# Kernel tuning notes

Measured on AMD Instinct MI355X. Metric: run time of the kernel, lower is better.

## Reference

```python
import jax, jax.numpy as jnp
import numpy as np

HEADS = 16
DIM_HEAD = 64

def setup_inputs() -> dict:
    key = jax.random.key(0)
    ks = jax.random.split(key, 7)
    B, Nq, Dq = 4, 2048, 1024
    Nk, Dc = 1024, 768
    inner = HEADS * DIM_HEAD  # 1024
    sq = 1.0 / np.sqrt(Dq)
    sc = 1.0 / np.sqrt(Dc)
    si = 1.0 / np.sqrt(inner)
    return {
        "x": jax.random.normal(ks[0], (B, Nq, Dq), dtype=jnp.float32),
        "context": jax.random.normal(ks[1], (B, Nk, Dc), dtype=jnp.float32),
        "Wq": jax.random.normal(ks[2], (Dq, inner), dtype=jnp.float32) * sq,
        "Wk": jax.random.normal(ks[3], (Dc, inner), dtype=jnp.float32) * sc,
        "Wv": jax.random.normal(ks[4], (Dc, inner), dtype=jnp.float32) * sc,
        "Wo": jax.random.normal(ks[5], (inner, Dq), dtype=jnp.float32) * si,
        "bo": jax.random.normal(ks[6], (Dq,), dtype=jnp.float32) * 0.01,
    }

def reference(x, context, Wq, Wk, Wv, Wo, bo):
    B, Nq, _ = x.shape
    Nk = context.shape[1]
    h, dh = HEADS, DIM_HEAD
    # projections (no bias on q/k/v, matching nn.Linear(bias=False))
    q = (x @ Wq).reshape(B, Nq, h, dh)        # [B,Nq,h,dh]
    k = (context @ Wk).reshape(B, Nk, h, dh)  # [B,Nk,h,dh]
    v = (context @ Wv).reshape(B, Nk, h, dh)
    scale = 1.0 / jnp.sqrt(jnp.asarray(dh, dtype=x.dtype))
    # scores: [B,h,Nq,Nk]
    scores = jnp.einsum('bqhd,bkhd->bhqk', q, k) * scale
    attn = jax.nn.softmax(scores, axis=-1)
    out = jnp.einsum('bhqk,bkhd->bqhd', attn, v).reshape(B, Nq, h * dh)
    return out @ Wo + bo
```

## Files before the change

kernel.cpp:

```cpp
#include <hip/hip_runtime.h>

typedef __bf16 bf16;
typedef __bf16 bf16x2 __attribute__((ext_vector_type(2)));
typedef __bf16 bf16x4 __attribute__((ext_vector_type(4)));
typedef __bf16 bf16x8 __attribute__((ext_vector_type(8)));
typedef float f32x4 __attribute__((ext_vector_type(4)));

#define MFMA(a, b, c) __builtin_amdgcn_mfma_f32_16x16x32_bf16(a, b, c, 0, 0, 0)

#define GLD16(gptr, ldsptr)                                                        \
  __builtin_amdgcn_global_load_lds(                                                \
      (const __attribute__((address_space(1))) unsigned int*)(gptr),               \
      (__attribute__((address_space(3))) unsigned int*)(ldsptr), 16, 0, 0)

union I4B8 { int4 i; bf16x8 v; };
union HI { bf16x2 h; int i; };

__global__ __launch_bounds__(256) void prep_k(const float* __restrict__ x, bf16* __restrict__ xb,
                                              const float* __restrict__ ctx, bf16* __restrict__ ctxb,
                                              const float* __restrict__ Wq, bf16* __restrict__ WqT,
                                              const float* __restrict__ Wk, bf16* __restrict__ WkvT,
                                              const float* __restrict__ Wv,
                                              const float* __restrict__ Wo, bf16* __restrict__ WoT) {
  __shared__ float t[32][33];
  const int bid = blockIdx.x;
  if (bid < 5632) {
    const float* in; bf16* out; size_t i;
    if (bid < 4096) { in = x; out = xb; i = ((size_t)bid * 256 + threadIdx.x) * 8; }
    else { in = ctx; out = ctxb; i = ((size_t)(bid - 4096) * 256 + threadIdx.x) * 8; }
    const float4 a = *(const float4*)(in + i);
    const float4 b = *(const float4*)(in + i + 4);
    bf16x8 o;
    o[0] = (bf16)a.x; o[1] = (bf16)a.y; o[2] = (bf16)a.z; o[3] = (bf16)a.w;
    o[4] = (bf16)b.x; o[5] = (bf16)b.y; o[6] = (bf16)b.z; o[7] = (bf16)b.w;
    *(bf16x8*)(out + i) = o;
    return;
  }
  const int tt = bid - 5632;
  const int z = tt >> 10, rem = tt & 1023;
  const float* in; bf16* out; int R; float sc = 1.0f;
  if (z == 0)      { in = Wq; out = WqT;                R = 1024; sc = 0.18033688f; }
  else if (z == 1) { in = Wk; out = WkvT;               R = 768; }
  else if (z == 2) { in = Wv; out = WkvT + 1024 * 768;  R = 768; }
  else             { in = Wo; out = WoT;                R = 1024; }
  const int c0 = (rem & 31) * 32, r0 = (rem >> 5) * 32;
  if (r0 >= R) return;
  const int tx = threadIdx.x & 31, ty = threadIdx.x >> 5;
#pragma unroll
  for (int i = 0; i < 4; i++)
    t[ty + i * 8][tx] = in[(size_t)(r0 + ty + i * 8) * 1024 + c0 + tx];
  __syncthreads();
#pragma unroll
  for (int i = 0; i < 4; i++)
    out[(size_t)(c0 + ty + i * 8) * R + r0 + tx] = (bf16)(t[tx][ty + i * 8] * sc);
}

__device__ __forceinline__ void ld_af(bf16x8 (&af)[4][2], const bf16* Ls, int base,
                                      int wm, int c, int q, int swz) {
#pragma unroll
  for (int mi = 0; mi < 4; mi++) {
    const int rr = wm * 64 + mi * 16 + c;
#pragma unroll
    for (int kk = 0; kk < 2; kk++)
      af[mi][kk] = *(const bf16x8*)&Ls[base + rr * 64 + ((kk * 32 + q * 8) ^ swz)];
  }
}
__device__ __forceinline__ void ld_bb(bf16x8 (&bb)[2][2], const bf16* Ls, int base,
                                      int wn, int c, int q, int swz) {
#pragma unroll
  for (int ni = 0; ni < 2; ni++) {
    const int rn = wn * 32 + ni * 16 + c;
#pragma unroll
    for (int kk = 0; kk < 2; kk++)
      bb[ni][kk] = *(const bf16x8*)&Ls[base + rn * 64 + ((kk * 32 + q * 8) ^ swz)];
  }
}
template <int MODE>
__device__ __forceinline__ void mma16(f32x4 (&pacc)[4][2], const bf16x8 (&af)[4][2],
                                      const bf16x8 (&bb)[2][2]) {
  __builtin_amdgcn_s_setprio(1);
#pragma unroll
  for (int mi = 0; mi < 4; mi++)
#pragma unroll
    for (int ni = 0; ni < 2; ni++)
#pragma unroll
      for (int kk = 0; kk < 2; kk++) {
        if constexpr (MODE == 2)
          pacc[mi][ni] = MFMA(af[mi][kk], bb[ni][kk], pacc[mi][ni]);
        else
          pacc[mi][ni] = MFMA(bb[ni][kk], af[mi][kk], pacc[mi][ni]);
      }
  __builtin_amdgcn_s_setprio(0);
}

template <int MODE>
__device__ __forceinline__ void gemm256(const bf16* __restrict__ A,
                                        const bf16* __restrict__ Bt,
                                        int K, int m0, int n0,
                                        void* __restrict__ C0,
                                        const float* __restrict__ bias,
                                        bf16* Ls) {
  const int tid = threadIdx.x;
  const int lane = tid & 63, w = tid >> 6;
  const int wm = w >> 2, wn = w & 3;
  const int q = lane >> 4, c = lane & 15;
  const int swz = (c & 7) * 8;

  const int rl = tid >> 3, seg = tid & 7;
  const bf16* Ag = A + (size_t)(m0 + rl) * K + ((seg ^ (rl & 7)) * 8);
  const bf16* Bg = Bt + (size_t)(n0 + rl) * K + ((seg ^ (rl & 7)) * 8);
  const size_t K64 = (size_t)K * 64, K128 = (size_t)K * 128;
  const int ws = w * 512;

  f32x4 acc[2][2][4][2] = {};

  GLD16(Ag,              &Ls[0 + ws]);
  GLD16(Ag + K64,        &Ls[4096 + ws]);
  GLD16(Ag + K128,       &Ls[8192 + ws]);
  GLD16(Ag + K128 + K64, &Ls[12288 + ws]);
  GLD16(Bg,              &Ls[32768 + ws]);
  GLD16(Bg + K64,        &Ls[32768 + 4096 + ws]);
  GLD16(Bg + K128,       &Ls[32768 + 8192 + ws]);
  GLD16(Bg + K128 + K64, &Ls[32768 + 12288 + ws]);

  int cur = 0;
  for (int k0 = 0; k0 < K; k0 += 64) {
    const int nxt = cur ^ 1;
    const size_t kn = (size_t)((k0 + 64 < K) ? k0 + 64 : k0);
    const int Ab = cur * 16384, Bb = 32768 + cur * 16384;
    const int An = nxt * 16384, Bn = 32768 + nxt * 16384;

    bf16x8 af[4][2], b0[2][2], b1[2][2];

    asm volatile("s_waitcnt vmcnt(2)" ::: "memory");
    asm volatile("s_barrier" ::: "memory");
    GLD16(Ag + kn,       &Ls[An + ws]);
    GLD16(Ag + kn + K64, &Ls[An + 4096 + ws]);
    ld_af(af, Ls, Ab, wm, c, q, swz);
    ld_bb(b0, Ls, Bb, wn, c, q, swz);
    mma16<MODE>(acc[0][0], af, b0);

    asm volatile("s_waitcnt vmcnt(2)" ::: "memory");
    asm volatile("s_barrier" ::: "memory");
    GLD16(Ag + kn + K128,       &Ls[An + 8192 + ws]);
    GLD16(Ag + kn + K128 + K64, &Ls[An + 12288 + ws]);
    ld_bb(b1, Ls, Bb + 8192, wn, c, q, swz);
    mma16<MODE>(acc[0][1], af, b1);

    asm volatile("s_barrier" ::: "memory");
    GLD16(Bg + kn,       &Ls[Bn + ws]);
    GLD16(Bg + kn + K64, &Ls[Bn + 4096 + ws]);
    ld_af(af, Ls, Ab + 8192, wm, c, q, swz);
    mma16<MODE>(acc[1][0], af, b0);

    asm volatile("s_barrier" ::: "memory");
    GLD16(Bg + kn + K128,       &Ls[Bn + 8192 + ws]);
    GLD16(Bg + kn + K128 + K64, &Ls[Bn + 12288 + ws]);
    mma16<MODE>(acc[1][1], af, b1);

    cur = nxt;
  }
  asm volatile("s_waitcnt vmcnt(0)" ::: "memory");

  if constexpr (MODE == 0 || MODE == 1) {
#pragma unroll
    for (int h = 0; h < 2; h++)
#pragma unroll
      for (int g = 0; g < 2; g++)
#pragma unroll
        for (int ni = 0; ni < 2; ni++) {
          const int col = n0 + g * 128 + wn * 32 + ni * 16 + q * 4;
          float4 bv4 = {};
          if constexpr (MODE == 1) bv4 = *(const float4*)&bias[col];
#pragma unroll
          for (int mi = 0; mi < 4; mi++) {
            const int row = m0 + h * 128 + wm * 64 + mi * 16 + c;
            if constexpr (MODE == 0) {
              bf16x4 vv;
#pragma unroll
              for (int r2 = 0; r2 < 4; r2++) vv[r2] = (bf16)acc[h][g][mi][ni][r2];
              *(bf16x4*)&((bf16*)C0)[(size_t)row * 1024 + col] = vv;
            } else {
              f32x4 vv;
              vv[0] = acc[h][g][mi][ni][0] + bv4.x; vv[1] = acc[h][g][mi][ni][1] + bv4.y;
              vv[2] = acc[h][g][mi][ni][2] + bv4.z; vv[3] = acc[h][g][mi][ni][3] + bv4.w;
              *(f32x4*)&((float*)C0)[(size_t)row * 1024 + col] = vv;
            }
          }
        }
  } else {
#pragma unroll
    for (int h = 0; h < 2; h++)
#pragma unroll
      for (int g = 0; g < 2; g++)
#pragma unroll
        for (int ni = 0; ni < 2; ni++) {
          const int col = n0 + g * 128 + wn * 32 + ni * 16 + c;
#pragma unroll
          for (int mi = 0; mi < 4; mi++) {
            const int rbase = m0 + h * 128 + wm * 64 + mi * 16 + q * 4;
            const int b = rbase >> 10, key = rbase & 1023;
            bf16* VT = (bf16*)C0;
            const int hh = col >> 6, d = col & 63;
            const int kl = key & 63;
            const int pkey = (key & ~63) | (kl & 32) | ((kl & 12) << 1) | ((kl & 16) >> 2);
            bf16x4 vv;
#pragma unroll
            for (int r2 = 0; r2 < 4; r2++) vv[r2] = (bf16)acc[h][g][mi][ni][r2];
            *(bf16x4*)&VT[((size_t)(b * 16 + hh) * 64 + d) * 1024 + pkey] = vv;
          }
        }
  }
}

__global__ __launch_bounds__(512) void proj_k(const bf16* __restrict__ xb,
                                              const bf16* __restrict__ ctxb,
                                              const bf16* __restrict__ WqT,
                                              const bf16* __restrict__ WkvT,
                                              bf16* __restrict__ Q,
                                              bf16* __restrict__ Kp,
                                              bf16* __restrict__ VT) {
  extern __shared__ __align__(16) bf16 Ls[];
  const int bid = blockIdx.x;
  if (bid < 128) {
    const int x = bid & 7, i = bid >> 3;
    const int rt = x * 4 + (i >> 2), ct = i & 3;
    gemm256<0>(xb, WqT, 1024, rt * 256, ct * 256, Q, nullptr, Ls);
  } else if (bid < 192) {
    const int t = bid - 128, x = t & 7, i = t >> 3;
    const int rt = x * 2 + (i >> 2), ct = i & 3;
    gemm256<0>(ctxb, WkvT, 768, rt * 256, ct * 256, Kp, nullptr, Ls);
  } else {
    const int t = bid - 192, x = t & 7, i = t >> 3;
    const int rt = x * 2 + (i >> 2), ct = i & 3;
    gemm256<2>(ctxb, WkvT + (size_t)1024 * 768, 768, rt * 256, ct * 256, VT, nullptr, Ls);
  }
}

__device__ __forceinline__ void gemm_body_out(const bf16* __restrict__ A,
                                              const bf16* __restrict__ Bt,
                                              int K, int m0, int n0,
                                              float* __restrict__ C0,
                                              const float* __restrict__ bias,
                                              bf16* As, bf16* Bs) {
  const int tid = threadIdx.x;
  const int lane = tid & 63, wave = tid >> 6;
  const int wm = wave >> 1, wn = wave & 1;
  const int q = lane >> 4, c = lane & 15;

  f32x4 acc[4][4] = {};
  const int r = tid >> 3;
  const int col8 = ((tid & 7) * 8) ^ ((r & 7) * 8);
  const bf16* Ag = A + (size_t)(m0 + r) * K + col8;
  const bf16* Bg = Bt + (size_t)(n0 + r) * K + col8;
  const size_t K32 = (size_t)K * 32;
  bf16* AsW = As + wave * 512;
  bf16* BsW = Bs + wave * 512;
  const int swz = (c & 7) * 8;

  for (int k0 = 0; k0 < K; k0 += 64) {
    __syncthreads();
    GLD16(Ag + k0,            AsW);
    GLD16(Ag + k0 + K32,      AsW + 2048);
    GLD16(Ag + k0 + 2 * K32,  AsW + 4096);
    GLD16(Ag + k0 + 3 * K32,  AsW + 6144);
    GLD16(Bg + k0,            BsW);
    GLD16(Bg + k0 + K32,      BsW + 2048);
    GLD16(Bg + k0 + 2 * K32,  BsW + 4096);
    GLD16(Bg + k0 + 3 * K32,  BsW + 6144);
    __syncthreads();
#pragma unroll
    for (int kk = 0; kk < 2; kk++) {
      const int cx = (kk * 32 + q * 8) ^ swz;
      bf16x8 af[4], bfr[4];
#pragma unroll
      for (int mi = 0; mi < 4; mi++)
        af[mi] = *(const bf16x8*)&As[(wm * 64 + mi * 16 + c) * 64 + cx];
#pragma unroll
      for (int ni = 0; ni < 4; ni++)
        bfr[ni] = *(const bf16x8*)&Bs[(wn * 64 + ni * 16 + c) * 64 + cx];
      __builtin_amdgcn_s_setprio(1);
#pragma unroll
      for (int mi = 0; mi < 4; mi++)
#pragma unroll
        for (int ni = 0; ni < 4; ni++)
          acc[mi][ni] = MFMA(bfr[ni], af[mi], acc[mi][ni]);
      __builtin_amdgcn_s_setprio(0);
    }
  }

#pragma unroll
  for (int ni = 0; ni < 4; ni++) {
    const int col = n0 + wn * 64 + ni * 16 + q * 4;
    float4 bv4 = *(const float4*)&bias[col];
#pragma unroll
    for (int mi = 0; mi < 4; mi++) {
      const int row = m0 + wm * 64 + mi * 16 + c;
      f32x4 vv;
      vv[0] = acc[mi][ni][0] + bv4.x; vv[1] = acc[mi][ni][1] + bv4.y;
      vv[2] = acc[mi][ni][2] + bv4.z; vv[3] = acc[mi][ni][3] + bv4.w;
      *(f32x4*)&C0[(size_t)row * 1024 + col] = vv;
    }
  }
}

__global__ __launch_bounds__(256) void out_k(const bf16* __restrict__ O,
                                             const bf16* __restrict__ WoT,
                                             float* __restrict__ out,
                                             const float* __restrict__ bo) {
  __shared__ __align__(16) bf16 As[8192];
  __shared__ __align__(16) bf16 Bs[8192];
  const int bid = blockIdx.x;
  const int s = (bid & 7) * 64 + (bid >> 3);
  gemm_body_out(O, WoT, 1024, (s >> 3) * 128, (s & 7) * 128, out, bo, As, Bs);
}

__global__ __launch_bounds__(256, 2) void attn_k(const bf16* __restrict__ Qg,
                                                 const bf16* __restrict__ Kg,
                                                 const bf16* __restrict__ VTg,
                                                 bf16* __restrict__ Og) {
  __shared__ __align__(16) bf16 Ks[2][64][64];
  __shared__ __align__(16) bf16 Vt[2][64][64];
  const int tid = threadIdx.x;
  const int lane = tid & 63, w = tid >> 6;
  const int q = lane >> 4, c = lane & 15;
  const int bid = blockIdx.x;
  const int pair = (bid & 7) * 8 + (bid >> 6);
  const int head = pair & 15, b = pair >> 4;
  const int q0 = ((bid >> 3) & 7) * 256;

  bf16x8 aQ[4][2];
#pragma unroll
  for (int mj = 0; mj < 4; mj++)
#pragma unroll
    for (int ks = 0; ks < 2; ks++)
      aQ[mj][ks] = *(const bf16x8*)(Qg + (size_t)(b * 2048 + q0 + w * 64 + mj * 16 + c) * 1024 +
                                    head * 64 + ks * 32 + q * 8);

  f32x4 o[4][4] = {};
  f32x4 ol[4] = {};
  bf16x8 vone;
#pragma unroll
  for (int i = 0; i < 8; i++) vone[i] = (bf16)1.0f;

  const int srow = tid >> 2, sc = tid & 3;
  const int ws0 = ((2 * sc) ^ (srow & 7)) * 8;
  const int ws1 = ((2 * sc + 1) ^ (srow & 7)) * 8;
  const int rsw = c & 7;
  const bf16* Kbase = Kg + (size_t)(b * 1024 + srow) * 1024 + head * 64 + sc * 16;
  const bf16* Vbase = VTg + ((size_t)(b * 16 + head) * 64 + srow) * 1024 + sc * 16;

  bf16x8 rk0 = *(const bf16x8*)(Kbase);
  bf16x8 rk1 = *(const bf16x8*)(Kbase + 8);
  bf16x8 rv0 = *(const bf16x8*)(Vbase);
  bf16x8 rv1 = *(const bf16x8*)(Vbase + 8);
  *(bf16x8*)&Ks[0][srow][ws0] = rk0;
  *(bf16x8*)&Ks[0][srow][ws1] = rk1;
  *(bf16x8*)&Vt[0][srow][ws0] = rv0;
  *(bf16x8*)&Vt[0][srow][ws1] = rv1;
  __syncthreads();

  for (int kt = 0; kt < 16; kt++) {
    const int cur = kt & 1, nxt = cur ^ 1;
    if (kt < 15) {
      const size_t ko = (size_t)(kt + 1) * 65536;
      const int vo = (kt + 1) * 64;
      rk0 = *(const bf16x8*)(Kbase + ko);
      rk1 = *(const bf16x8*)(Kbase + ko + 8);
      rv0 = *(const bf16x8*)(Vbase + vo);
      rv1 = *(const bf16x8*)(Vbase + vo + 8);
    }

    f32x4 st[4][4] = {};
#pragma unroll
    for (int ks = 0; ks < 2; ks++) {
      bf16x8 ak[4];
#pragma unroll
      for (int ni = 0; ni < 4; ni++)
        ak[ni] = *(const bf16x8*)&Ks[cur][ni * 16 + c][((ks * 4 + q) ^ rsw) * 8];
      __builtin_amdgcn_s_setprio(1);
#pragma unroll
      for (int mj = 0; mj < 4; mj++)
#pragma unroll
        for (int ni = 0; ni < 4; ni++)
          st[mj][ni] = MFMA(ak[ni], aQ[mj][ks], st[mj][ni]);
      __builtin_amdgcn_s_setprio(0);
    }

    int pk[4][4][2];
#pragma unroll
    for (int mj = 0; mj < 4; mj++)
#pragma unroll
      for (int ni = 0; ni < 4; ni++) {
        float p0 = __builtin_amdgcn_exp2f(st[mj][ni][0]);
        float p1 = __builtin_amdgcn_exp2f(st[mj][ni][1]);
        float p2 = __builtin_amdgcn_exp2f(st[mj][ni][2]);
        float p3 = __builtin_amdgcn_exp2f(st[mj][ni][3]);
        HI h0, h1;
        h0.h[0] = (bf16)p0; h0.h[1] = (bf16)p1;
        h1.h[0] = (bf16)p2; h1.h[1] = (bf16)p3;
        pk[mj][ni][0] = h0.i;
        pk[mj][ni][1] = h1.i;
      }

#pragma unroll
    for (int ks2 = 0; ks2 < 2; ks2++) {
      bf16x8 bv[4];
#pragma unroll
      for (int ni = 0; ni < 4; ni++)
        bv[ni] = *(const bf16x8*)&Vt[cur][ni * 16 + c][((ks2 * 4 + q) ^ rsw) * 8];
#pragma unroll
      for (int mi = 0; mi < 4; mi++) {
        I4B8 pa;
        pa.i.x = pk[mi][2 * ks2][0];
        pa.i.y = pk[mi][2 * ks2][1];
        pa.i.z = pk[mi][2 * ks2 + 1][0];
        pa.i.w = pk[mi][2 * ks2 + 1][1];
        __builtin_amdgcn_s_setprio(1);
#pragma unroll
        for (int ni = 0; ni < 4; ni++)
          o[mi][ni] = MFMA(pa.v, bv[ni], o[mi][ni]);
        ol[mi] = MFMA(pa.v, vone, ol[mi]);
        __builtin_amdgcn_s_setprio(0);
      }
    }

    if (kt < 15) {
      *(bf16x8*)&Ks[nxt][srow][ws0] = rk0;
      *(bf16x8*)&Ks[nxt][srow][ws1] = rk1;
      *(bf16x8*)&Vt[nxt][srow][ws0] = rv0;
      *(bf16x8*)&Vt[nxt][srow][ws1] = rv1;
    }
    __syncthreads();
  }

#pragma unroll
  for (int mi = 0; mi < 4; mi++) {
    float inv[4];
#pragma unroll
    for (int r = 0; r < 4; r++) inv[r] = 1.0f / ol[mi][r];
#pragma unroll
    for (int ni = 0; ni < 4; ni++)
#pragma unroll
      for (int r = 0; r < 4; r++) {
        const int qrow = q0 + w * 64 + mi * 16 + q * 4 + r;
        const int col = head * 64 + ni * 16 + c;
        Og[(size_t)(b * 2048 + qrow) * 1024 + col] = (bf16)(o[mi][ni][r] * inv[r]);
      }
  }
}

extern "C" void kernel_launch(void* const* d_in, const int* in_sizes, int n_in,
                              void* d_out, int out_size, void* d_ws, size_t ws_size,
                              hipStream_t stream) {
  (void)in_sizes; (void)n_in; (void)out_size; (void)ws_size;
  const float* x   = (const float*)d_in[0];
  const float* ctx = (const float*)d_in[1];
  const float* Wq  = (const float*)d_in[2];
  const float* Wk  = (const float*)d_in[3];
  const float* Wv  = (const float*)d_in[4];
  const float* Wo  = (const float*)d_in[5];
  const float* bo  = (const float*)d_in[6];
  float* out = (float*)d_out;

  char* ws = (char*)d_ws;
  const size_t MB = 1u << 20;
  bf16* WqT  = (bf16*)(ws);
  bf16* WkvT = (bf16*)(ws + 2 * MB);
  bf16* WoT  = (bf16*)(ws + 5 * MB);
  bf16* ctxb = (bf16*)(ws + 7 * MB);
  bf16* xb   = (bf16*)(ws + 13 * MB);
  bf16* Q    = (bf16*)(ws + 29 * MB);
  bf16* Kp   = (bf16*)(ws + 45 * MB);
  bf16* VT   = (bf16*)(ws + 53 * MB);
  bf16* O    = xb;

  prep_k<<<5632 + 4096, 256, 0, stream>>>(x, xb, ctx, ctxb, Wq, WqT, Wk, WkvT, Wv, Wo, WoT);

  proj_k<<<256, 512, 131072, stream>>>(xb, ctxb, WqT, WkvT, Q, Kp, VT);

  attn_k<<<512, 256, 0, stream>>>(Q, Kp, VT, O);

  out_k<<<512, 256, 0, stream>>>(O, WoT, out, bo);
}
```

Baseline: 205.0 us.

## Software-pipeline attention loop so QK of next tile overlaps PV of previous

Restructures the attention K/V loop into a prologue, a steady state and an epilogue. Each iteration computes QK^T scores for tile kt while running the PV MFMAs for tile kt-1 using probabilities packed in the previous iteration. K/V shared memory moves from double to triple buffering to keep the previous V tile resident. The aim is to overlap the exp/convert VALU work with MFMA work instead of serializing them. In exchange, the scores and packed probabilities are live at the same time, which raises register pressure. LDS usage also grows, and the loop now uses runtime modulo buffer indices.

```diff
diff --git a/kernel.cpp b/kernel.cpp
--- a/kernel.cpp
+++ b/kernel.cpp
@@ -319,8 +319,8 @@
                                                  const bf16* __restrict__ Kg,
                                                  const bf16* __restrict__ VTg,
                                                  bf16* __restrict__ Og) {
-  __shared__ __align__(16) bf16 Ks[2][64][64];
-  __shared__ __align__(16) bf16 Vt[2][64][64];
+  __shared__ __align__(16) bf16 Ks[3][64][64];
+  __shared__ __align__(16) bf16 Vt[3][64][64];
   const int tid = threadIdx.x;
   const int lane = tid & 63, w = tid >> 6;
   const int q = lane >> 4, c = lane & 15;
@@ -358,26 +358,21 @@
   *(bf16x8*)&Ks[0][srow][ws1] = rk1;
   *(bf16x8*)&Vt[0][srow][ws0] = rv0;
   *(bf16x8*)&Vt[0][srow][ws1] = rv1;
+  rk0 = *(const bf16x8*)(Kbase + 65536);
+  rk1 = *(const bf16x8*)(Kbase + 65536 + 8);
+  rv0 = *(const bf16x8*)(Vbase + 64);
+  rv1 = *(const bf16x8*)(Vbase + 64 + 8);
   __syncthreads();
 
-  for (int kt = 0; kt < 16; kt++) {
-    const int cur = kt & 1, nxt = cur ^ 1;
-    if (kt < 15) {
-      const size_t ko = (size_t)(kt + 1) * 65536;
-      const int vo = (kt + 1) * 64;
-      rk0 = *(const bf16x8*)(Kbase + ko);
-      rk1 = *(const bf16x8*)(Kbase + ko + 8);
-      rv0 = *(const bf16x8*)(Vbase + vo);
-      rv1 = *(const bf16x8*)(Vbase + vo + 8);
-    }
-
+  int pk[4][4][2];
+  {
     f32x4 st[4][4] = {};
 #pragma unroll
     for (int ks = 0; ks < 2; ks++) {
       bf16x8 ak[4];
 #pragma unroll
       for (int ni = 0; ni < 4; ni++)
-        ak[ni] = *(const bf16x8*)&Ks[cur][ni * 16 + c][((ks * 4 + q) ^ rsw) * 8];
+        ak[ni] = *(const bf16x8*)&Ks[0][ni * 16 + c][((ks * 4 + q) ^ rsw) * 8];
       __builtin_amdgcn_s_setprio(1);
 #pragma unroll
       for (int mj = 0; mj < 4; mj++)
@@ -386,8 +381,6 @@
           st[mj][ni] = MFMA(ak[ni], aQ[mj][ks], st[mj][ni]);
       __builtin_amdgcn_s_setprio(0);
     }
-
-    int pk[4][4][2];
 #pragma unroll
     for (int mj = 0; mj < 4; mj++)
 #pragma unroll
@@ -402,13 +395,49 @@
         pk[mj][ni][0] = h0.i;
         pk[mj][ni][1] = h1.i;
       }
+  }
+  *(bf16x8*)&Ks[1][srow][ws0] = rk0;
+  *(bf16x8*)&Ks[1][srow][ws1] = rk1;
+  *(bf16x8*)&Vt[1][srow][ws0] = rv0;
+  *(bf16x8*)&Vt[1][srow][ws1] = rv1;
+  __syncthreads();
+
+#pragma unroll 1
+  for (int kt = 1; kt < 16; kt++) {
+    const int cur = kt % 3;
+    const int prv = (kt + 2) % 3;
+    const int nb  = (kt + 1) % 3;
+    if (kt < 15) {
+      const size_t ko = (size_t)(kt + 1) * 65536;
+      const int vo = (kt + 1) * 64;
+      rk0 = *(const bf16x8*)(Kbase + ko);
+      rk1 = *(const bf16x8*)(Kbase + ko + 8);
+      rv0 = *(const bf16x8*)(Vbase + vo);
+      rv1 = *(const bf16x8*)(Vbase + vo + 8);
+    }
+
+    f32x4 st[4][4] = {};
+#pragma unroll
+    for (int ks = 0; ks < 2; ks++) {
+      bf16x8 ak[4];
+#pragma unroll
+      for (int ni = 0; ni < 4; ni++)
+        ak[ni] = *(const bf16x8*)&Ks[cur][ni * 16 + c][((ks * 4 + q) ^ rsw) * 8];
+      __builtin_amdgcn_s_setprio(1);
+#pragma unroll
+      for (int mj = 0; mj < 4; mj++)
+#pragma unroll
+        for (int ni = 0; ni < 4; ni++)
+          st[mj][ni] = MFMA(ak[ni], aQ[mj][ks], st[mj][ni]);
+      __builtin_amdgcn_s_setprio(0);
+    }
 
 #pragma unroll
     for (int ks2 = 0; ks2 < 2; ks2++) {
       bf16x8 bv[4];
 #pragma unroll
       for (int ni = 0; ni < 4; ni++)
-        bv[ni] = *(const bf16x8*)&Vt[cur][ni * 16 + c][((ks2 * 4 + q) ^ rsw) * 8];
+        bv[ni] = *(const bf16x8*)&Vt[prv][ni * 16 + c][((ks2 * 4 + q) ^ rsw) * 8];
 #pragma unroll
       for (int mi = 0; mi < 4; mi++) {
         I4B8 pa;
@@ -425,13 +454,48 @@
       }
     }
 
+#pragma unroll
+    for (int mj = 0; mj < 4; mj++)
+#pragma unroll
+      for (int ni = 0; ni < 4; ni++) {
+        float p0 = __builtin_amdgcn_exp2f(st[mj][ni][0]);
+        float p1 = __builtin_amdgcn_exp2f(st[mj][ni][1]);
+        float p2 = __builtin_amdgcn_exp2f(st[mj][ni][2]);
+        float p3 = __builtin_amdgcn_exp2f(st[mj][ni][3]);
+        HI h0, h1;
+        h0.h[0] = (bf16)p0; h0.h[1] = (bf16)p1;
+        h1.h[0] = (bf16)p2; h1.h[1] = (bf16)p3;
+        pk[mj][ni][0] = h0.i;
+        pk[mj][ni][1] = h1.i;
+      }
+
     if (kt < 15) {
-      *(bf16x8*)&Ks[nxt][srow][ws0] = rk0;
-      *(bf16x8*)&Ks[nxt][srow][ws1] = rk1;
-      *(bf16x8*)&Vt[nxt][srow][ws0] = rv0;
-      *(bf16x8*)&Vt[nxt][srow][ws1] = rv1;
+      *(bf16x8*)&Ks[nb][srow][ws0] = rk0;
+      *(bf16x8*)&Ks[nb][srow][ws1] = rk1;
+      *(bf16x8*)&Vt[nb][srow][ws0] = rv0;
+      *(bf16x8*)&Vt[nb][srow][ws1] = rv1;
     }
     __syncthreads();
+  }
+
+#pragma unroll
+  for (int ks2 = 0; ks2 < 2; ks2++) {
+    bf16x8 bv[4];
+#pragma unroll
+    for (int ni = 0; ni < 4; ni++)
+      bv[ni] = *(const bf16x8*)&Vt[0][ni * 16 + c][((ks2 * 4 + q) ^ rsw) * 8];
+#pragma unroll
+    for (int mi = 0; mi < 4; mi++) {
+      I4B8 pa;
+      pa.i.x = pk[mi][2 * ks2][0];
+      pa.i.y = pk[mi][2 * ks2][1];
+      pa.i.z = pk[mi][2 * ks2 + 1][0];
+      pa.i.w = pk[mi][2 * ks2 + 1][1];
+#pragma unroll
+      for (int ni = 0; ni < 4; ni++)
+        o[mi][ni] = MFMA(pa.v, bv[ni], o[mi][ni]);
+      ol[mi] = MFMA(pa.v, vone, ol[mi]);
+    }
   }
 
 #pragma unroll
```

Measured after the change: 230.7 us. +12.6%, slower.
